# Kernel optimization log

Measured on AMD Instinct MI355X. Metric: run time of the kernel, lower is better.

Reference implementation:

```python
import jax, jax.numpy as jnp
import numpy as np

ADAPTER_SCALAR = 0.1
LN_EPS = 1e-5
BN_EPS = 1e-5


def setup_inputs() -> dict:
    key = jax.random.key(0)
    ks = jax.random.split(key, 4)
    B, S, H, D, K = 8, 4096, 8, 128, 32
    x = jax.random.normal(ks[0], (B, S, H * D), dtype=jnp.float32)
    # down/up proj weights init with std=0.01, biases zero (per init_weights)
    w_down = 0.01 * jax.random.normal(ks[1], (H, D, K), dtype=jnp.float32)
    w_up = 0.01 * jax.random.normal(ks[2], (H, K, D), dtype=jnp.float32)
    return {
        "x": x,
        "ln_gamma": jnp.ones((H, D), jnp.float32),
        "ln_beta": jnp.zeros((H, D), jnp.float32),
        "w_down": w_down,
        "b_down": jnp.zeros((H, K), jnp.float32),
        "w_up": w_up,
        "b_up": jnp.zeros((H, D), jnp.float32),
        "bn_gamma": jnp.ones((H, D), jnp.float32),
        "bn_beta": jnp.zeros((H, D), jnp.float32),
    }


def reference(x, ln_gamma, ln_beta, w_down, b_down, w_up, b_up, bn_gamma, bn_beta):
    B, S, _ = x.shape
    H, D, K = w_down.shape
    xh = x.reshape(B, S, H, D)  # per-head slices
    residual = xh
    # LayerNorm over head_dim (per head affine)
    mu = jnp.mean(xh, axis=-1, keepdims=True)
    var = jnp.mean(jnp.square(xh - mu), axis=-1, keepdims=True)
    h = (xh - mu) * jax.lax.rsqrt(var + LN_EPS) * ln_gamma + ln_beta
    # down proj -> GELU (exact) -> up proj, grouped over heads
    h = jnp.einsum("bshd,hdk->bshk", h, w_down) + b_down
    h = jax.nn.gelu(h, approximate=False)
    h = jnp.einsum("bshk,hkd->bshd", h, w_up) + b_up
    # BatchNorm1d (training mode): batch stats over flattened (B*S) per head per feature
    bmu = jnp.mean(h, axis=(0, 1), keepdims=True)
    bvar = jnp.mean(jnp.square(h - bmu), axis=(0, 1), keepdims=True)  # biased var
    h = (h - bmu) * jax.lax.rsqrt(bvar + BN_EPS) * bn_gamma + bn_beta
    out = ADAPTER_SCALAR * h + residual
    return out.reshape(B, S, H * D)
```

## Files before the change

### kernel.cpp

```cpp
#include <hip/hip_runtime.h>
#include <math.h>

#define NB 8
#define NS 4096
#define NH 8
#define ND 128
#define NK 32
#define NT (NB*NS)
#define HD (NH*ND)

#define LN_EPS_F 1e-5f
#define BN_EPS_F 1e-5f
#define ADAPTER_SCALE 0.1f

#define THREADS 256
#define NWAVES 4
#define BPH 128
#define NBLK (NH*BPH)
#define TILES_PER_WAVE 4

typedef short short8 __attribute__((ext_vector_type(8)));
typedef float f32x4 __attribute__((ext_vector_type(4)));

__device__ inline unsigned short f2bf(float f) {
    union { float f; unsigned u; } v; v.f = f;
    unsigned r = v.u + 0x7fffu + ((v.u >> 16) & 1u);
    return (unsigned short)(r >> 16);
}

__global__ void zero_kernel(float* p, int n) {
    int i = blockIdx.x * blockDim.x + threadIdx.x;
    if (i < n) p[i] = 0.0f;
}

template <int MODE>
__global__ __launch_bounds__(THREADS, 4)
void adapter_mfma(const float* __restrict__ x,
                  const float* __restrict__ ln_g, const float* __restrict__ ln_b,
                  const float* __restrict__ w_down, const float* __restrict__ b_down,
                  const float* __restrict__ w_up, const float* __restrict__ b_up,
                  float* __restrict__ gsum, float* __restrict__ gssq,
                  const float* __restrict__ avec, const float* __restrict__ cvec,
                  float* __restrict__ out)
{
    __shared__ __align__(16) unsigned short s_xn[NWAVES][16*136];
    __shared__ __align__(16) unsigned short s_gl[NWAVES][16*40];
    __shared__ float s_stats[2][ND];

    const int h    = blockIdx.x & 7;
    const int bidx = blockIdx.x >> 3;
    const int tid  = threadIdx.x;
    const int wave = tid >> 6;
    const int lane = tid & 63;
    const int lg   = lane >> 4;
    const int lc   = lane & 15;

    if constexpr (MODE == 0) {
        if (tid < ND) { s_stats[0][tid] = 0.f; s_stats[1][tid] = 0.f; }
        __syncthreads();
    }

    short8 wd[4][2];
    #pragma unroll
    for (int s = 0; s < 4; ++s)
        #pragma unroll
        for (int nt = 0; nt < 2; ++nt)
            #pragma unroll
            for (int i = 0; i < 8; ++i)
                wd[s][nt][i] = (short)f2bf(w_down[h*ND*NK + (32*s + 8*lg + i)*NK + 16*nt + lc]);
    short8 wu[8];
    #pragma unroll
    for (int nt = 0; nt < 8; ++nt)
        #pragma unroll
        for (int i = 0; i < 8; ++i)
            wu[nt][i] = (short)f2bf(w_up[h*NK*ND + (8*lg + i)*ND + 16*nt + lc]);

    float bdreg[2];
    #pragma unroll
    for (int nt = 0; nt < 2; ++nt) bdreg[nt] = b_down[h*NK + 16*nt + lc];
    float bupreg[8];
    #pragma unroll
    for (int nt = 0; nt < 8; ++nt) bupreg[nt] = b_up[h*ND + 16*nt + lc];

    float areg[8], cfold[8];
    if constexpr (MODE == 1) {
        #pragma unroll
        for (int nt = 0; nt < 8; ++nt) {
            areg[nt]  = avec[h*ND + 16*nt + lc];
            cfold[nt] = fmaf(areg[nt], bupreg[nt], cvec[h*ND + 16*nt + lc]);
        }
    }

    const float2 lng2 = *(const float2*)(ln_g + h*ND + 2*lane);
    const float2 lnb2 = *(const float2*)(ln_b + h*ND + 2*lane);

    float sumacc[8], ssqacc[8];
    #pragma unroll
    for (int nt = 0; nt < 8; ++nt) { sumacc[nt] = 0.f; ssqacc[nt] = 0.f; }

    for (int it = 0; it < TILES_PER_WAVE; ++it) {
        const int tbase = bidx*256 + (wave + NWAVES*it)*16;

        for (int t = 0; t < 16; ++t) {
            const float2 v = *(const float2*)(x + (size_t)(tbase + t)*HD + h*ND + 2*lane);
            float s1 = v.x + v.y;
            float s2 = v.x*v.x + v.y*v.y;
            #pragma unroll
            for (int off = 32; off; off >>= 1) { s1 += __shfl_xor(s1, off); s2 += __shfl_xor(s2, off); }
            const float mu   = s1 * (1.0f/ND);
            const float rstd = rsqrtf(s2*(1.0f/ND) - mu*mu + LN_EPS_F);
            const float xa = (v.x - mu)*rstd*lng2.x + lnb2.x;
            const float xb = (v.y - mu)*rstd*lng2.y + lnb2.y;
            const unsigned pack = (unsigned)f2bf(xa) | ((unsigned)f2bf(xb) << 16);
            *(unsigned*)&s_xn[wave][t*136 + 2*lane] = pack;
        }
        __builtin_amdgcn_wave_barrier();

        short8 ax[4];
        #pragma unroll
        for (int s = 0; s < 4; ++s)
            ax[s] = *(const short8*)&s_xn[wave][lc*136 + 32*s + 8*lg];

        #pragma unroll
        for (int nt = 0; nt < 2; ++nt) {
            f32x4 acc = {0.f, 0.f, 0.f, 0.f};
            #pragma unroll
            for (int s = 0; s < 4; ++s)
                acc = __builtin_amdgcn_mfma_f32_16x16x32_bf16(ax[s], wd[s][nt], acc, 0, 0, 0);
            #pragma unroll
            for (int r = 0; r < 4; ++r) {
                const float vv = acc[r] + bdreg[nt];
                const float ge = 0.5f*vv*(1.0f + erff(vv*0.70710678118654752f));
                s_gl[wave][(4*lg + r)*40 + 16*nt + lc] = f2bf(ge);
            }
        }
        __builtin_amdgcn_wave_barrier();

        const short8 ag = *(const short8*)&s_gl[wave][lc*40 + 8*lg];
        #pragma unroll
        for (int nt = 0; nt < 8; ++nt) {
            f32x4 c2 = __builtin_amdgcn_mfma_f32_16x16x32_bf16(ag, wu[nt], (f32x4){0.f,0.f,0.f,0.f}, 0, 0, 0);
            if constexpr (MODE == 0) {
                #pragma unroll
                for (int r = 0; r < 4; ++r) {
                    const float hv = c2[r] + bupreg[nt];
                    sumacc[nt] += hv;
                    ssqacc[nt]  = fmaf(hv, hv, ssqacc[nt]);
                }
            } else {
                #pragma unroll
                for (int r = 0; r < 4; ++r) {
                    const size_t idx = (size_t)(tbase + 4*lg + r)*HD + h*ND + 16*nt + lc;
                    out[idx] = fmaf(areg[nt], c2[r], cfold[nt] + x[idx]);
                }
            }
        }
        __builtin_amdgcn_wave_barrier();
    }

    if constexpr (MODE == 0) {
        #pragma unroll
        for (int nt = 0; nt < 8; ++nt) {
            atomicAdd(&s_stats[0][16*nt + lc], sumacc[nt]);
            atomicAdd(&s_stats[1][16*nt + lc], ssqacc[nt]);
        }
        __syncthreads();
        if (tid < ND) {
            atomicAdd(gsum + h*ND + tid, s_stats[0][tid]);
            atomicAdd(gssq + h*ND + tid, s_stats[1][tid]);
        }
    }
}

__global__ void finalize_kernel(const float* __restrict__ gsum, const float* __restrict__ gssq,
                                const float* __restrict__ bn_g, const float* __restrict__ bn_b,
                                float* __restrict__ avec, float* __restrict__ cvec)
{
    const int i = blockIdx.x * blockDim.x + threadIdx.x;
    if (i < HD) {
        const float inv_n = 1.0f / (float)NT;
        const float mean = gsum[i] * inv_n;
        const float var  = gssq[i] * inv_n - mean*mean;
        const float rs   = rsqrtf(var + BN_EPS_F);
        const float a    = ADAPTER_SCALE * bn_g[i] * rs;
        avec[i] = a;
        cvec[i] = ADAPTER_SCALE * bn_b[i] - mean * a;
    }
}

extern "C" void kernel_launch(void* const* d_in, const int* in_sizes, int n_in,
                              void* d_out, int out_size, void* d_ws, size_t ws_size,
                              hipStream_t stream) {
    const float* x      = (const float*)d_in[0];
    const float* ln_g   = (const float*)d_in[1];
    const float* ln_b   = (const float*)d_in[2];
    const float* w_down = (const float*)d_in[3];
    const float* b_down = (const float*)d_in[4];
    const float* w_up   = (const float*)d_in[5];
    const float* b_up   = (const float*)d_in[6];
    const float* bn_g   = (const float*)d_in[7];
    const float* bn_b   = (const float*)d_in[8];
    float* out = (float*)d_out;

    float* ws   = (float*)d_ws;
    float* gsum = ws;
    float* gssq = ws + HD;
    float* avec = ws + 2*HD;
    float* cvec = ws + 3*HD;

    zero_kernel<<<(2*HD + 255)/256, 256, 0, stream>>>(gsum, 2*HD);
    adapter_mfma<0><<<NBLK, THREADS, 0, stream>>>(
        x, ln_g, ln_b, w_down, b_down, w_up, b_up,
        gsum, gssq, nullptr, nullptr, nullptr);
    finalize_kernel<<<(HD + 255)/256, 256, 0, stream>>>(gsum, gssq, bn_g, bn_b, avec, cvec);
    adapter_mfma<1><<<NBLK, THREADS, 0, stream>>>(
        x, ln_g, ln_b, w_down, b_down, w_up, b_up,
        nullptr, nullptr, avec, cvec, out);
}
```

Measured before the change: 381.8 us.

## Load x directly in MFMA operand layout and drop LDS staging of normalized rows

Each lane now loads 32 contiguous floats of one token row with vector loads, laid out to match the MFMA A operand. LayerNorm statistics are reduced with two cross-lane shuffles instead of a full six-step reduction for every token. This removes the per-token serial loop, the LDS round trip for normalized activations and the shuffle-heavy reductions. The grid is doubled, with half as many tiles per wave, and LN gamma/beta now come from LDS. The cost is more registers for the x tile and possibly fewer coalesced global loads.

After: 474.8 us. 24.4% more time.

```diff
diff --git a/kernel.cpp b/kernel.cpp
--- a/kernel.cpp
+++ b/kernel.cpp
@@ -15,9 +15,9 @@
 
 #define THREADS 256
 #define NWAVES 4
-#define BPH 128
+#define BPH 256
 #define NBLK (NH*BPH)
-#define TILES_PER_WAVE 4
+#define TPW 2
 
 typedef short short8 __attribute__((ext_vector_type(8)));
 typedef float f32x4 __attribute__((ext_vector_type(4)));
@@ -43,8 +43,9 @@
                   const float* __restrict__ avec, const float* __restrict__ cvec,
                   float* __restrict__ out)
 {
-    __shared__ __align__(16) unsigned short s_xn[NWAVES][16*136];
     __shared__ __align__(16) unsigned short s_gl[NWAVES][16*40];
+    __shared__ __align__(16) float s_lng[ND];
+    __shared__ __align__(16) float s_lnb[ND];
     __shared__ float s_stats[2][ND];
 
     const int h    = blockIdx.x & 7;
@@ -55,10 +56,9 @@
     const int lg   = lane >> 4;
     const int lc   = lane & 15;
 
-    if constexpr (MODE == 0) {
-        if (tid < ND) { s_stats[0][tid] = 0.f; s_stats[1][tid] = 0.f; }
-        __syncthreads();
-    }
+    if (tid < ND) { s_lng[tid] = ln_g[h*ND + tid]; s_lnb[tid] = ln_b[h*ND + tid]; }
+    else if (MODE == 0 && tid < 2*ND) { s_stats[0][tid - ND] = 0.f; s_stats[1][tid - ND] = 0.f; }
+    __syncthreads();
 
     short8 wd[4][2];
     #pragma unroll
@@ -91,35 +91,50 @@
         }
     }
 
-    const float2 lng2 = *(const float2*)(ln_g + h*ND + 2*lane);
-    const float2 lnb2 = *(const float2*)(ln_b + h*ND + 2*lane);
-
     float sumacc[8], ssqacc[8];
     #pragma unroll
     for (int nt = 0; nt < 8; ++nt) { sumacc[nt] = 0.f; ssqacc[nt] = 0.f; }
 
-    for (int it = 0; it < TILES_PER_WAVE; ++it) {
-        const int tbase = bidx*256 + (wave + NWAVES*it)*16;
-
-        for (int t = 0; t < 16; ++t) {
-            const float2 v = *(const float2*)(x + (size_t)(tbase + t)*HD + h*ND + 2*lane);
-            float s1 = v.x + v.y;
-            float s2 = v.x*v.x + v.y*v.y;
-            #pragma unroll
-            for (int off = 32; off; off >>= 1) { s1 += __shfl_xor(s1, off); s2 += __shfl_xor(s2, off); }
-            const float mu   = s1 * (1.0f/ND);
-            const float rstd = rsqrtf(s2*(1.0f/ND) - mu*mu + LN_EPS_F);
-            const float xa = (v.x - mu)*rstd*lng2.x + lnb2.x;
-            const float xb = (v.y - mu)*rstd*lng2.y + lnb2.y;
-            const unsigned pack = (unsigned)f2bf(xa) | ((unsigned)f2bf(xb) << 16);
-            *(unsigned*)&s_xn[wave][t*136 + 2*lane] = pack;
-        }
-        __builtin_amdgcn_wave_barrier();
+    for (int it = 0; it < TPW; ++it) {
+        const int tbase = bidx*128 + (wave + NWAVES*it)*16;
+
+        const float* xrow = x + (size_t)(tbase + lc)*HD + h*ND + 8*lg;
+        f32x4 xv[4][2];
+        #pragma unroll
+        for (int s = 0; s < 4; ++s) {
+            xv[s][0] = *(const f32x4*)(xrow + 32*s);
+            xv[s][1] = *(const f32x4*)(xrow + 32*s + 4);
+        }
+
+        float s1 = 0.f, s2 = 0.f;
+        #pragma unroll
+        for (int s = 0; s < 4; ++s)
+            #pragma unroll
+            for (int hf = 0; hf < 2; ++hf)
+                #pragma unroll
+                for (int j = 0; j < 4; ++j) {
+                    const float v = xv[s][hf][j];
+                    s1 += v;
+                    s2 = fmaf(v, v, s2);
+                }
+        s1 += __shfl_xor(s1, 16);  s2 += __shfl_xor(s2, 16);
+        s1 += __shfl_xor(s1, 32);  s2 += __shfl_xor(s2, 32);
+        const float mu   = s1 * (1.0f/ND);
+        const float rstd = rsqrtf(s2*(1.0f/ND) - mu*mu + LN_EPS_F);
 
         short8 ax[4];
         #pragma unroll
         for (int s = 0; s < 4; ++s)
-            ax[s] = *(const short8*)&s_xn[wave][lc*136 + 32*s + 8*lg];
+            #pragma unroll
+            for (int hf = 0; hf < 2; ++hf) {
+                const f32x4 gv = *(const f32x4*)&s_lng[32*s + 8*lg + 4*hf];
+                const f32x4 bv = *(const f32x4*)&s_lnb[32*s + 8*lg + 4*hf];
+                #pragma unroll
+                for (int j = 0; j < 4; ++j) {
+                    const float f = (xv[s][hf][j] - mu)*rstd*gv[j] + bv[j];
+                    ax[s][4*hf + j] = (short)f2bf(f);
+                }
+            }
 
         #pragma unroll
         for (int nt = 0; nt < 2; ++nt) {
```
